# Kernel tuning notes

Hardware: AMD Instinct MI355X
Metric: run time of the kernel (lower is better)

## Reference

```python
import jax, jax.numpy as jnp
import numpy as np

FEATURE_DIM = 512
NUM_HEADS = 8
HEAD_DIM = FEATURE_DIM // NUM_HEADS


def setup_inputs() -> dict:
    key = jax.random.key(0)
    ks = jax.random.split(key, 16)
    B, N, F = 16, 768, FEATURE_DIM
    Nb = N // 3
    s = 1.0 / np.sqrt(F)
    inp = {
        "x_1": jax.random.normal(ks[0], (B, N, F), jnp.float32),
        "x_2": jax.random.normal(ks[1], (B, N, F), jnp.float32),
        "z_b": jax.random.normal(ks[2], (Nb, F), jnp.float32),
        # weights stored [in, out] (torch Linear applies x @ W.T)
        "Wqkv_i": jax.random.normal(ks[3], (F, 3 * F), jnp.float32) * s,
        "Wqkv_j": jax.random.normal(ks[4], (F, 3 * F), jnp.float32) * s,
        "Wqkv_b": jax.random.normal(ks[5], (F, 3 * F), jnp.float32) * s,
        "W_f": jax.random.normal(ks[6], (2 * F, F), jnp.float32) * s,
        "b_f": jnp.zeros((F,), jnp.float32),
        "W_m": jax.random.normal(ks[7], (F, F), jnp.float32) * s,
        "b_m": jnp.zeros((F,), jnp.float32),
        "W_QKV": jax.random.normal(ks[8], (F, 3 * F), jnp.float32) * s,
        "W_proj": jax.random.normal(ks[9], (F, F), jnp.float32) * s,
        "b_proj": jnp.zeros((F,), jnp.float32),
    }
    return inp


def reference(x_1, x_2, z_b, Wqkv_i, Wqkv_j, Wqkv_b, W_f, b_f, W_m, b_m, W_QKV, W_proj, b_proj):
    z_i, z_j = x_1, x_2
    B, N, F = z_i.shape
    Nb = z_b.shape[0]
    scale = F ** -0.5           # full-dim attention scale
    Scale = HEAD_DIM ** -0.5    # multi-head attention scale

    zb = jnp.broadcast_to((z_b * 0.2)[None], (B, Nb, F))

    def split_qkv(x, W):
        qkv = (x @ W).reshape(x.shape[0], x.shape[1], 3, F)
        return qkv[:, :, 0], qkv[:, :, 1], qkv[:, :, 2]

    _, k_i, v_i = split_qkv(z_i, Wqkv_i)
    q_j, _, _ = split_qkv(z_j, Wqkv_j)
    q_b, k_b, v_b = split_qkv(zb, Wqkv_b)

    # bottleneck cross attentions (single-head, full feature dim)
    a_ib = jax.nn.softmax(jnp.einsum('bmf,bnf->bmn', q_b, k_i) * scale, axis=-1)  # [B,Nb,N]
    a_bj = jax.nn.softmax(jnp.einsum('bnf,bmf->bnm', q_j, k_b) * scale, axis=-1)  # [B,N,Nb]

    a_ib = jnp.einsum('bmn,bnf->bmf', a_ib, v_i)  # [B,Nb,F]
    attn_up = jax.nn.softmax(jnp.einsum('bnf,bmf->bnm', z_i, a_ib) * scale, axis=-1)  # [B,N,Nb]
    a_ib = jnp.einsum('bnm,bmf->bnf', attn_up, a_ib)  # [B,N,F]
    a_bj = jnp.einsum('bnm,bmf->bnf', a_bj, v_b)      # [B,N,F]
    a_ij = (a_ib + a_bj) * 0.5

    # gated fusion
    f_ij = jax.nn.sigmoid(jnp.concatenate([a_ij, z_j], axis=-1) @ W_f + b_f)
    h_ij = jax.nn.relu(z_i + (a_ij @ W_m + b_m) * f_ij)

    # standard multi-head self-attention
    QKV = (h_ij @ W_QKV).reshape(B, N, 3, NUM_HEADS, HEAD_DIM)
    Q, K, V = [jnp.transpose(QKV[:, :, t], (0, 2, 1, 3)) for t in range(3)]  # [B,H,N,hd]
    Attn = jax.nn.softmax(jnp.einsum('bhnd,bhmd->bhnm', Q, K) * Scale, axis=-1)
    H = jnp.einsum('bhnm,bhmd->bhnd', Attn, V)
    H = jnp.transpose(H, (0, 2, 1, 3)).reshape(B, N, F)
    return H @ W_proj + b_proj
```

## Files before the change

kernel.cpp:

```cpp
#include <hip/hip_runtime.h>
#include <hip/hip_bf16.h>

typedef __attribute__((ext_vector_type(8))) short short8;
typedef __attribute__((ext_vector_type(4))) float f32x4;
typedef __hip_bfloat16 bf16;
typedef unsigned short ushort;

__device__ __forceinline__ ushort f2b(float v) {
    bf16 h = __float2bfloat16(v);
    return *reinterpret_cast<ushort*>(&h);
}
__device__ __forceinline__ float b2f(ushort u) {
    return __uint_as_float((unsigned)u << 16);
}

#define GLD16(lds, gp) __builtin_amdgcn_global_load_lds( \
    (const __attribute__((address_space(1))) void*)(gp), \
    (__attribute__((address_space(3))) void*)(lds), 16, 0, 0)

__device__ __forceinline__ void xcd_swizzle(int& bx, int& by) {
    if (gridDim.z == 1 && (gridDim.y & 7) == 0) {
        const int id = bx + gridDim.x * by;
        const int xcd = id & 7, slot = id >> 3;
        by = xcd * (gridDim.y >> 3) + slot / gridDim.x;
        bx = slot - (slot / gridDim.x) * gridDim.x;
    }
}

template<typename OutT, int EPI, int TM>
__global__ __launch_bounds__(256) void gemm_bf16(
    const bf16* __restrict__ A, const bf16* __restrict__ B, OutT* __restrict__ C,
    int K, int lda, int ldb, int ldc, long sA, long sB, long sC,
    float alpha, const float* __restrict__ bias,
    int lda2, long sA2, int eld, long sE,
    bf16* __restrict__ px, bf16* __restrict__ py)
{
    constexpr int RT = TM / 32;
    constexpr int PLA = TM * 32;
    constexpr int PLB = 128 * 32;
    constexpr int NP = (TM == 64) ? 4 : 2;
    __shared__ __align__(16) bf16 As[NP * PLA];
    __shared__ __align__(16) bf16 Bs[NP * PLB];

    const int t = threadIdx.x;
    const int w = t >> 6, lane = t & 63;
    const int wr = w >> 1, wc = w & 1;
    const int lr = lane & 15, kc4 = lane >> 4;
    const int qr = lane >> 2;
    const int kcr = ((lane & 3) - ((lane >> 3) & 3)) & 3;
    int bx = blockIdx.x, by = blockIdx.y;
    xcd_swizzle(bx, by);
    const int row0 = by * TM, col0 = bx * 128;
    const int bz = blockIdx.z;

    const bf16* Asel = A; const bf16* Bsel = B;
    int abz = bz; long sBe = sB, sAe = sA; int ldbe = ldb, ldae = lda;
    if constexpr (EPI == 7) {
        if (bz >= 16) {
            Asel = (const bf16*)px; Bsel = (const bf16*)py;
            abz = bz - 16; sBe = 0; ldbe = eld; ldae = lda2; sAe = sA2;
        }
    }
    const bf16* Ab = Asel + (size_t)abz * sAe + (size_t)row0 * ldae;
    const bf16* Bb = Bsel + (size_t)abz * sBe + (size_t)col0 * ldbe;

    const bf16* ga0; const bf16* ga1 = nullptr;
    if constexpr (TM == 64) {
        ga0 = Ab + (size_t)(w * 16 + qr) * ldae + kcr * 8;
    } else {
        ga0 = Ab + (size_t)(w * 32 + qr) * ldae + kcr * 8;
        ga1 = Ab + (size_t)(w * 32 + 16 + qr) * ldae + kcr * 8;
    }
    const bf16* gb0 = Bb + (size_t)(w * 32 + qr) * ldbe + kcr * 8;
    const bf16* gb1 = Bb + (size_t)(w * 32 + 16 + qr) * ldbe + kcr * 8;
    bf16* lA0; bf16* lA1 = nullptr;
    if constexpr (TM == 64) { lA0 = &As[w * 512]; }
    else                    { lA0 = &As[w * 1024]; lA1 = &As[w * 1024 + 512]; }
    bf16* lB0 = &Bs[w * 1024];
    bf16* lB1 = &Bs[w * 1024 + 512];

    f32x4 acc[RT][4] = {};

    const int cSw = ((kc4 + ((lr >> 1) & 3)) & 3) * 8;
    const bf16* ApBase = &As[(wr * (TM / 2) + lr) * 32 + cSw];
    const bf16* BpBase = &Bs[(wc * 64 + lr) * 32 + cSw];

    auto stageP = [&](int plane, int ko) {
        GLD16(lA0 + plane * PLA, ga0 + ko);
        if constexpr (TM == 128) GLD16(lA1 + plane * PLA, ga1 + ko);
        GLD16(lB0 + plane * PLB, gb0 + ko);
        GLD16(lB1 + plane * PLB, gb1 + ko);
    };
    auto compP = [&](int plane) {
        const bf16* Ap = ApBase + plane * PLA;
        const bf16* Bp = BpBase + plane * PLB;
        short8 af[RT], bfr[4];
#pragma unroll
        for (int i = 0; i < RT; ++i) af[i]  = *(const short8*)(Ap + i * 512);
#pragma unroll
        for (int j = 0; j < 4; ++j) bfr[j] = *(const short8*)(Bp + j * 512);
#pragma unroll
        for (int i = 0; i < RT; ++i)
#pragma unroll
            for (int j = 0; j < 4; ++j)
                acc[i][j] = __builtin_amdgcn_mfma_f32_16x16x32_bf16(af[i], bfr[j], acc[i][j], 0, 0, 0);
    };

    if constexpr (TM == 64) {
        stageP(0, 0); stageP(1, 32);
        int buf = 0;
        for (int k0 = 0; k0 < K; k0 += 64) {
            __syncthreads();
            if (k0 + 64 < K) {
                stageP((buf ^ 1) * 2,     k0 + 64);
                stageP((buf ^ 1) * 2 + 1, k0 + 96);
            }
            compP(buf * 2); compP(buf * 2 + 1);
            buf ^= 1;
        }
    } else {
        stageP(0, 0);
        int buf = 0;
        for (int k0 = 0; k0 < K; k0 += 32) {
            __syncthreads();
            if (k0 + 32 < K) stageP(buf ^ 1, k0 + 32);
            compP(buf);
            buf ^= 1;
        }
    }

    if constexpr (EPI == 4) {
        const int sec = bx >> 2;
        const int h0 = (bx & 3) * 2;
        const int b  = by / 6;
        const int n0 = (by % 6) * TM;
        bf16* dq = (bf16*)C;
#pragma unroll
        for (int j = 0; j < 4; ++j) {
            const int col = wc * 64 + j * 16 + lr;
            const int h = h0 + (col >> 6), hd = col & 63;
            const size_t bh = (size_t)b * 8 + h;
#pragma unroll
            for (int i = 0; i < RT; ++i) {
                const int n = n0 + wr * (TM / 2) + i * 16 + kc4 * 4;
                if (sec == 2) {
                    __align__(8) ushort o[4];
#pragma unroll
                    for (int r = 0; r < 4; ++r) o[r] = f2b(acc[i][j][r]);
                    *(int2*)&py[(bh * 64 + hd) * 768 + n] = *(const int2*)o;
                } else {
                    bf16* d = (sec == 0) ? dq : px;
#pragma unroll
                    for (int r = 0; r < 4; ++r)
                        d[(bh * 768 + n + r) * 64 + hd] = __float2bfloat16(acc[i][j][r]);
                }
            }
        }
        return;
    } else if constexpr (EPI == 5) {
        const int b  = by / 6;
        const int n0 = (by % 6) * TM;
#pragma unroll
        for (int j = 0; j < 4; ++j) {
            const int col = col0 + wc * 64 + j * 16 + lr;
#pragma unroll
            for (int i = 0; i < RT; ++i) {
                const int n = n0 + wr * (TM / 2) + i * 16 + kc4 * 4;
                if (col < 512) {
#pragma unroll
                    for (int r = 0; r < 4; ++r)
                        ((bf16*)C)[((size_t)b * 768 + n + r) * 512 + col] = __float2bfloat16(acc[i][j][r]);
                } else {
                    __align__(8) ushort o[4];
#pragma unroll
                    for (int r = 0; r < 4; ++r) o[r] = f2b(acc[i][j][r]);
                    *(int2*)&py[((size_t)b * 512 + (col - 512)) * 768 + n] = *(const int2*)o;
                }
            }
        }
        return;
    }

    OutT* Cb = C + (size_t)bz * sC;
#pragma unroll
    for (int j = 0; j < 4; ++j) {
        const int col = col0 + wc * 64 + j * 16 + lr;
        const float bv = bias ? bias[col] : 0.f;
#pragma unroll
        for (int i = 0; i < RT; ++i) {
            const int rb = row0 + wr * (TM / 2) + i * 16 + kc4 * 4;
            if constexpr (EPI == 6) {
                __align__(8) ushort o[4];
#pragma unroll
                for (int r = 0; r < 4; ++r) {
                    o[r] = f2b(alpha * acc[i][j][r]);
                    Cb[(size_t)(rb + r) * ldc + col] = __float2bfloat16(alpha * acc[i][j][r]);
                }
                *(int2*)&py[(size_t)bz * sE + (size_t)col * eld + rb] = *(const int2*)o;
            } else {
#pragma unroll
                for (int r = 0; r < 4; ++r) {
                    const int row = rb + r;
                    float v = alpha * acc[i][j][r] + bv;
                    if constexpr (sizeof(OutT) == 2)
                        Cb[(size_t)row * ldc + col] = __float2bfloat16(v);
                    else
                        Cb[(size_t)row * ldc + col] = v;
                }
            }
        }
    }
}

__global__ __launch_bounds__(256) void gemm_gate(
    const bf16* __restrict__ A, const bf16* __restrict__ Bf,
    const bf16* __restrict__ Bm, bf16* __restrict__ Cout,
    const float* __restrict__ bias_f, const float* __restrict__ bias_m,
    const float* __restrict__ x1)
{
    constexpr int AHW = 64 * 32;
    constexpr int BHW = 128 * 32;
    __shared__ __align__(16) bf16 As[2 * AHW];
    __shared__ __align__(16) bf16 FsS[2 * BHW];
    __shared__ __align__(16) bf16 MsS[2 * BHW];

    const int t = threadIdx.x;
    const int w = t >> 6, lane = t & 63;
    const int wr = w >> 1, wc = w & 1;
    const int lr = lane & 15, kc4 = lane >> 4;
    const int qr = lane >> 2;
    const int kcr = ((lane & 3) - ((lane >> 3) & 3)) & 3;
    int bx = blockIdx.x, by = blockIdx.y;
    xcd_swizzle(bx, by);
    const int row0 = by * 64, col0 = bx * 128;

    const bf16* ga0 = A  + (size_t)(row0 + w * 16 + qr) * 1024 + kcr * 8;
    const bf16* gf0 = Bf + (size_t)(col0 + w * 32 + qr) * 1024 + kcr * 8;
    const bf16* gf1 = Bf + (size_t)(col0 + w * 32 + 16 + qr) * 1024 + kcr * 8;
    const bf16* gm0 = Bm + (size_t)(col0 + w * 32 + qr) * 512 + kcr * 8;
    const bf16* gm1 = Bm + (size_t)(col0 + w * 32 + 16 + qr) * 512 + kcr * 8;
    bf16* lA0 = &As[w * 512];
    bf16* lF0 = &FsS[w * 1024]; bf16* lF1 = &FsS[w * 1024 + 512];
    bf16* lM0 = &MsS[w * 1024]; bf16* lM1 = &MsS[w * 1024 + 512];

    f32x4 acc1[2][4] = {};
    f32x4 acc2[2][4] = {};

    const int cSw = ((kc4 + ((lr >> 1) & 3)) & 3) * 8;
    const bf16* ApBase = &As[(wr * 32 + lr) * 32 + cSw];
    const bf16* FpBase = &FsS[(wc * 64 + lr) * 32 + cSw];
    const bf16* MpBase = &MsS[(wc * 64 + lr) * 32 + cSw];

    GLD16(lA0, ga0);
    GLD16(lF0, gf0); GLD16(lF1, gf1);
    GLD16(lM0, gm0); GLD16(lM1, gm1);

    auto step = [&](int kk, int rd, int st) {
        __syncthreads();
        const int kn = kk + 32;
        if (kn < 1024) {
            GLD16(lA0 + st * AHW, ga0 + kn);
            GLD16(lF0 + st * BHW, gf0 + kn);
            GLD16(lF1 + st * BHW, gf1 + kn);
            if (kn < 512) {
                GLD16(lM0 + st * BHW, gm0 + kn);
                GLD16(lM1 + st * BHW, gm1 + kn);
            }
        }
        const bf16* Ap = ApBase + rd * AHW;
        const bf16* Fp = FpBase + rd * BHW;
        short8 af[2], ff[4];
#pragma unroll
        for (int i = 0; i < 2; ++i) af[i] = *(const short8*)(Ap + i * 512);
#pragma unroll
        for (int j = 0; j < 4; ++j) ff[j] = *(const short8*)(Fp + j * 512);
#pragma unroll
        for (int i = 0; i < 2; ++i)
#pragma unroll
            for (int j = 0; j < 4; ++j)
                acc1[i][j] = __builtin_amdgcn_mfma_f32_16x16x32_bf16(af[i], ff[j], acc1[i][j], 0, 0, 0);
        if (kk < 512) {
            const bf16* Mp = MpBase + rd * BHW;
            short8 mf[4];
#pragma unroll
            for (int j = 0; j < 4; ++j) mf[j] = *(const short8*)(Mp + j * 512);
#pragma unroll
            for (int i = 0; i < 2; ++i)
#pragma unroll
                for (int j = 0; j < 4; ++j)
                    acc2[i][j] = __builtin_amdgcn_mfma_f32_16x16x32_bf16(af[i], mf[j], acc2[i][j], 0, 0, 0);
        }
    };

    for (int k0 = 0; k0 < 1024; k0 += 64) {
        step(k0, 0, 1);
        step(k0 + 32, 1, 0);
    }

#pragma unroll
    for (int j = 0; j < 4; ++j) {
        const int col = col0 + wc * 64 + j * 16 + lr;
        const float bvf = bias_f[col], bvm = bias_m[col];
#pragma unroll
        for (int i = 0; i < 2; ++i) {
            const int rb = row0 + wr * 32 + i * 16 + kc4 * 4;
#pragma unroll
            for (int r = 0; r < 4; ++r) {
                const int row = rb + r;
                const float sig = 1.f / (1.f + __expf(-(acc1[i][j][r] + bvf)));
                const float rr = x1[(size_t)row * 512 + col] + (acc2[i][j][r] + bvm) * sig;
                Cout[(size_t)row * 512 + col] = __float2bfloat16(rr > 0.f ? rr : 0.f);
            }
        }
    }
}

template<typename TI, int NSRC>
__global__ __launch_bounds__(256) void k_transpose(
    const TI* __restrict__ s0, const TI* __restrict__ s1,
    const TI* __restrict__ s2, const TI* __restrict__ s3,
    bf16* __restrict__ dst, int src_ld, int dst_ld, long sSrc, long sDst,
    int rep, long repStride)
{
    __shared__ float tile[64][65];
    const int t = threadIdx.x;
    const int c0 = blockIdx.x * 64, r0 = blockIdx.y * 64;
    const int z = blockIdx.z;
    const TI* src = s0;
    if (NSRC > 1) src = (z == 0) ? s0 : (z == 1) ? s1 : (z == 2) ? s2 : s3;
    {
        const int r = t >> 2, cq = (t & 3) * 16;
        const TI* sp = src + (size_t)z * sSrc + (size_t)(r0 + r) * src_ld + c0 + cq;
        if constexpr (sizeof(TI) == 4) {
#pragma unroll
            for (int u = 0; u < 16; u += 4) {
                float4 v = *(const float4*)((const float*)sp + u);
                tile[r][cq + u]     = v.x; tile[r][cq + u + 1] = v.y;
                tile[r][cq + u + 2] = v.z; tile[r][cq + u + 3] = v.w;
            }
        } else {
            const ushort* up = (const ushort*)sp;
            union { short8 v; ushort u[8]; } p0, p1;
            p0.v = *(const short8*)up; p1.v = *(const short8*)(up + 8);
#pragma unroll
            for (int u = 0; u < 8; ++u) {
                tile[r][cq + u]     = b2f(p0.u[u]);
                tile[r][cq + 8 + u] = b2f(p1.u[u]);
            }
        }
    }
    __syncthreads();
    const int c = t >> 2, rq = (t & 3) * 16;
    __align__(16) ushort ob[16];
#pragma unroll
    for (int u = 0; u < 16; ++u) ob[u] = f2b(tile[rq + u][c]);
    for (int rp = 0; rp < rep; ++rp) {
        bf16* dp = dst + (size_t)rp * repStride + (size_t)z * sDst + (size_t)(c0 + c) * dst_ld + r0 + rq;
        *(int4*)dp       = *(const int4*)&ob[0];
        *(int4*)(dp + 8) = *(const int4*)&ob[8];
    }
}

__global__ __launch_bounds__(256) void k_cast3(const float* __restrict__ x1,
    const float* __restrict__ x2, const float* __restrict__ zb,
    const float* __restrict__ wj,
    bf16* __restrict__ d1, bf16* __restrict__ d2, bf16* __restrict__ d3,
    bf16* __restrict__ d4)
{
    const int z = blockIdx.z;
    const float* src; bf16* dst; int ld; float scale; int n;
    if (z == 0)      { src = x1; dst = d1; ld = 512;  scale = 1.f;  n = 6291456; }
    else if (z == 1) { src = x2; dst = d2; ld = 1024; scale = 1.f;  n = 6291456; }
    else if (z == 2) { src = zb; dst = d3; ld = 512;  scale = 0.2f; n = 131072;  }
    else             { src = wj; dst = d4; ld = 512;  scale = 1.f;  n = 262144;  }
    int i = (blockIdx.x * 256 + threadIdx.x) * 8;
    if (i >= n) return;
    int si = i;
    if (z == 3) si = (i >> 9) * 1536 + (i & 511);
    float4 a = *(const float4*)(src + si), b = *(const float4*)(src + si + 4);
    __align__(16) ushort o[8];
    o[0] = f2b(a.x * scale); o[1] = f2b(a.y * scale); o[2] = f2b(a.z * scale); o[3] = f2b(a.w * scale);
    o[4] = f2b(b.x * scale); o[5] = f2b(b.y * scale); o[6] = f2b(b.z * scale); o[7] = f2b(b.w * scale);
    int row = i >> 9, col = i & 511;
    *(int4*)(dst + (size_t)row * ld + col) = *(const int4*)o;
}

template<int COLS, int MODE>
__global__ __launch_bounds__(256) void softmax_wave(const float* __restrict__ X,
                                                    bf16* __restrict__ Y)
{
    const int wv = threadIdx.x >> 6, lane = threadIdx.x & 63;
    const long row = (long)blockIdx.x * 4 + wv;
    const float* src = X + row * COLS;
    constexpr int V = COLS / 64;
    float v[V];
#pragma unroll
    for (int i = 0; i < V; ++i) v[i] = src[lane + i * 64];
    float m = v[0];
#pragma unroll
    for (int i = 1; i < V; ++i) m = fmaxf(m, v[i]);
#pragma unroll
    for (int o = 32; o; o >>= 1) m = fmaxf(m, __shfl_xor(m, o));
    float s = 0.f;
#pragma unroll
    for (int i = 0; i < V; ++i) { v[i] = __expf(v[i] - m); s += v[i]; }
#pragma unroll
    for (int o = 32; o; o >>= 1) s += __shfl_xor(s, o);
    const float inv = 1.f / s;
    bf16* dst;
    if constexpr (MODE == 0) {
        dst = Y + row * COLS;
    } else {
        const int z = (int)(row / 768), mm = (int)(row % 768);
        dst = Y + ((size_t)(z & 15) * 768 + mm) * 512 + (z >> 4) * 256;
    }
#pragma unroll
    for (int i = 0; i < V; ++i) dst[lane + i * 64] = __float2bfloat16(v[i] * inv);
}

__global__ __launch_bounds__(256) void mhsa_flash_mfma(
    const bf16* __restrict__ Qb, const bf16* __restrict__ Kb,
    const bf16* __restrict__ VT, bf16* __restrict__ Hout)
{
    constexpr int LD = 72;
    __shared__ __align__(16) ushort Qs[64 * LD];
    __shared__ __align__(16) ushort Ks[64 * LD];
    __shared__ __align__(16) ushort Vt[64 * LD];
    __shared__ __align__(16) ushort Ps[64 * LD];

    const int t = threadIdx.x;
    const int w = t >> 6, lane = t & 63;
    const int l16 = lane & 15, q4 = lane >> 4;
    const int h = blockIdx.x, b = blockIdx.y, qt = blockIdx.z;
    const size_t bh = (size_t)b * 8 + h;
    const ushort* qbase = (const ushort*)Qb + bh * 768 * 64;
    const ushort* kbase = (const ushort*)Kb + bh * 768 * 64;
    const ushort* vbase = (const ushort*)VT + bh * 64 * 768;

    const int r = t >> 2, c0 = (t & 3) * 16;

    {
        const ushort* src = qbase + (size_t)(qt * 64 + r) * 64 + c0;
        *(int4*)&Qs[r * LD + c0]     = *(const int4*)src;
        *(int4*)&Qs[r * LD + c0 + 8] = *(const int4*)(src + 8);
    }

    int4 ka0, ka1, va0, va1;
    {
        const ushort* ks = kbase + (size_t)r * 64 + c0;
        ka0 = *(const int4*)ks; ka1 = *(const int4*)(ks + 8);
        const ushort* vs = vbase + (size_t)r * 768 + c0;
        va0 = *(const int4*)vs; va1 = *(const int4*)(vs + 8);
    }
    __syncthreads();

    short8 qf0 = *(const short8*)&Qs[(w * 16 + l16) * LD + q4 * 8];
    short8 qf1 = *(const short8*)&Qs[(w * 16 + l16) * LD + 32 + q4 * 8];

    float lsum[4] = {0.f, 0.f, 0.f, 0.f};
    f32x4 acc[4] = {};

    for (int kt = 0; kt < 12; ++kt) {
        if (kt) __syncthreads();
        *(int4*)&Ks[r * LD + c0]     = ka0;
        *(int4*)&Ks[r * LD + c0 + 8] = ka1;
        *(int4*)&Vt[r * LD + c0]     = va0;
        *(int4*)&Vt[r * LD + c0 + 8] = va1;
        __syncthreads();

        if (kt < 11) {
            const ushort* ks = kbase + (size_t)((kt + 1) * 64 + r) * 64 + c0;
            ka0 = *(const int4*)ks; ka1 = *(const int4*)(ks + 8);
            const ushort* vs = vbase + (size_t)r * 768 + (kt + 1) * 64 + c0;
            va0 = *(const int4*)vs; va1 = *(const int4*)(vs + 8);
        }

        f32x4 s[4] = {};
#pragma unroll
        for (int nt = 0; nt < 4; ++nt) {
            short8 kf0 = *(const short8*)&Ks[(nt * 16 + l16) * LD + q4 * 8];
            short8 kf1 = *(const short8*)&Ks[(nt * 16 + l16) * LD + 32 + q4 * 8];
            s[nt] = __builtin_amdgcn_mfma_f32_16x16x32_bf16(qf0, kf0, s[nt], 0, 0, 0);
            s[nt] = __builtin_amdgcn_mfma_f32_16x16x32_bf16(qf1, kf1, s[nt], 0, 0, 0);
        }

#pragma unroll
        for (int nt = 0; nt < 4; ++nt) {
#pragma unroll
            for (int e = 0; e < 4; ++e) {
                const float p = __expf(s[nt][e] * 0.125f);
                lsum[e] += p;
                Ps[(w * 16 + q4 * 4 + e) * LD + nt * 16 + l16] = f2b(p);
            }
        }

        short8 pf0 = *(const short8*)&Ps[(w * 16 + l16) * LD + q4 * 8];
        short8 pf1 = *(const short8*)&Ps[(w * 16 + l16) * LD + 32 + q4 * 8];
#pragma unroll
        for (int jt = 0; jt < 4; ++jt) {
            short8 vf0 = *(const short8*)&Vt[(jt * 16 + l16) * LD + q4 * 8];
            short8 vf1 = *(const short8*)&Vt[(jt * 16 + l16) * LD + 32 + q4 * 8];
            acc[jt] = __builtin_amdgcn_mfma_f32_16x16x32_bf16(pf0, vf0, acc[jt], 0, 0, 0);
            acc[jt] = __builtin_amdgcn_mfma_f32_16x16x32_bf16(pf1, vf1, acc[jt], 0, 0, 0);
        }
    }

    const int orow = qt * 64 + w * 16 + q4 * 4;
#pragma unroll
    for (int e = 0; e < 4; ++e) {
        float l = lsum[e];
        l += __shfl_xor(l, 1);
        l += __shfl_xor(l, 2);
        l += __shfl_xor(l, 4);
        l += __shfl_xor(l, 8);
        const float inv = 1.f / l;
        const size_t rbase = ((size_t)b * 768 + orow + e) * 512 + h * 64;
#pragma unroll
        for (int jt = 0; jt < 4; ++jt)
            Hout[rbase + jt * 16 + l16] = __float2bfloat16(acc[jt][e] * inv);
    }
}

extern "C" void kernel_launch(void* const* d_in, const int* in_sizes, int n_in,
                              void* d_out, int out_size, void* d_ws, size_t ws_size,
                              hipStream_t stream)
{
    (void)in_sizes; (void)n_in; (void)out_size; (void)ws_size;
    const float* x1     = (const float*)d_in[0];
    const float* x2     = (const float*)d_in[1];
    const float* z_b    = (const float*)d_in[2];
    const float* Wqkv_i = (const float*)d_in[3];
    const float* Wqkv_j = (const float*)d_in[4];
    const float* Wqkv_b = (const float*)d_in[5];
    const float* W_f    = (const float*)d_in[6];
    const float* b_f    = (const float*)d_in[7];
    const float* W_m    = (const float*)d_in[8];
    const float* b_m    = (const float*)d_in[9];
    const float* W_QKV  = (const float*)d_in[10];
    const float* W_proj = (const float*)d_in[11];
    const float* b_proj = (const float*)d_in[12];
    float* out = (float*)d_out;

    const float scale = 0.044194173824159216f;

    char* base = (char*)d_ws;
    size_t off = 0;
    auto alloc = [&](size_t bytes) { char* r = base + off; off += (bytes + 255) & ~(size_t)255; return r; };

    char* Rq  = alloc((size_t)3 * 25165824);
    char* R1  = Rq;
    char* R2  = Rq + 25165824;
    char* R3  = Rq + 2 * 25165824;
    char* R4  = alloc(25165824);
    bf16* Wt4     = (bf16*)alloc((size_t)3 * 1536 * 512 * 2);
    bf16* Wt_f    = (bf16*)alloc(512 * 1024 * 2);
    bf16* Wt_mp   = (bf16*)alloc((size_t)2 * 512 * 512 * 2);
    bf16* Wj_bf   = (bf16*)alloc(512 * 512 * 2);
    bf16* Gbuf    = (bf16*)alloc(256 * 512 * 2);
    bf16* c_zb    = (bf16*)alloc(256 * 512 * 2);
    bf16* qkvb    = (bf16*)alloc(256 * 1536 * 2);
    bf16* aib0    = (bf16*)alloc((size_t)16 * 256 * 512 * 2);
    bf16* Bcat    = (bf16*)alloc((size_t)16 * 512 * 512 * 2);
    float* S      = (float*)alloc((size_t)32 * 768 * 256 * 4);
    bf16* Sb1     = (bf16*)alloc((size_t)16 * 256 * 768 * 2);
    bf16* Sb_cat  = (bf16*)alloc((size_t)16 * 768 * 512 * 2);
    bf16* c_cat   = (bf16*)alloc((size_t)12288 * 1024 * 2);
    bf16* hbuf    = (bf16*)alloc((size_t)12288 * 512 * 2);

    bf16* Wt_i = Wt4, *Wt_b = Wt4 + 1536 * 512,
        *Wt_qkv = Wt4 + (size_t)2 * 1536 * 512;
    bf16* Wt_m = Wt_mp, *Wt_proj = Wt_mp + 512 * 512;

    bf16*  Kc   = (bf16*)R1;
    bf16*  Qb   = (bf16*)R1;
    bf16*  Kb   = (bf16*)(R1 + 12582912);
    bf16*  v_iT = (bf16*)R2;
    bf16*  VTb  = (bf16*)R2;
    bf16*  c_x1 = (bf16*)R3;
    bf16*  Hout = (bf16*)R4;

    auto G64 = [&](const bf16* A, const bf16* B, void* C, bool outBf,
                   int M, int N, int K, int lda, int ldb, int ldc,
                   long sA, long sB, long sC, int batch, float alpha, const float* bias) {
        dim3 grid(N / 128, M / 64, batch);
        if (outBf) gemm_bf16<bf16, 0, 64><<<grid, 256, 0, stream>>>(A, B, (bf16*)C, K, lda, ldb, ldc, sA, sB, sC, alpha, bias, 0, 0, 0, 0, nullptr, nullptr);
        else       gemm_bf16<float, 0, 64><<<grid, 256, 0, stream>>>(A, B, (float*)C, K, lda, ldb, ldc, sA, sB, sC, alpha, bias, 0, 0, 0, 0, nullptr, nullptr);
    };

    k_cast3<<<dim3(3072, 1, 4), 256, 0, stream>>>(x1, x2, z_b, Wqkv_j,
                                                  c_x1, c_cat + 512, c_zb, Wj_bf);
    k_transpose<float, 3><<<dim3(24, 8, 3), 256, 0, stream>>>(
        Wqkv_i, Wqkv_b, W_QKV, nullptr, Wt4, 1536, 512, 0, 1536L * 512, 1, 0);
    k_transpose<float, 1><<<dim3(8, 16, 1), 256, 0, stream>>>(
        W_f, nullptr, nullptr, nullptr, Wt_f, 512, 1024, 0, 0, 1, 0);
    k_transpose<float, 2><<<dim3(8, 8, 2), 256, 0, stream>>>(
        W_m, W_proj, nullptr, nullptr, Wt_mp, 512, 512, 0, 512L * 512, 1, 0);

    G64(c_zb, Wt_b, qkvb, true, 256, 1536, 512, 512, 512, 1536, 0, 0, 0, 1, 1.f, nullptr);
    G64(qkvb + 512, Wj_bf, Gbuf, true, 256, 512, 512, 1536, 512, 512, 0, 0, 0, 1, 1.f, nullptr);
    k_transpose<bf16, 1><<<dim3(8, 4, 1), 256, 0, stream>>>(
        qkvb + 1024, nullptr, nullptr, nullptr, Bcat + 256, 1536, 512, 0, 0, 16, 512L * 512);
    gemm_bf16<bf16, 5, 128><<<dim3(8, 96, 1), 256, 0, stream>>>(
        c_x1, Wt_i + 512 * 512, Kc, 512, 512, 512, 512, 0, 0, 0,
        1.f, nullptr, 0, 0, 0, 0, nullptr, v_iT);
    G64(qkvb, Kc, S, false, 256, 768, 512, 1536, 512, 768, 0, 768L * 512, 256L * 768, 16, scale, nullptr);
    softmax_wave<768, 0><<<1024, 256, 0, stream>>>(S, Sb1);
    gemm_bf16<bf16, 6, 64><<<dim3(4, 4, 16), 256, 0, stream>>>(
        Sb1, v_iT, aib0, 768, 768, 768, 512, 256L * 768, 512L * 768, 256L * 512,
        1.f, nullptr, 0, 0, 512, 512L * 512, nullptr, Bcat);
    gemm_bf16<float, 7, 64><<<dim3(2, 12, 32), 256, 0, stream>>>(
        c_x1, aib0, S, 512, 512, 512, 256, 768L * 512, 256L * 512, 768L * 256,
        scale, nullptr, 1024, 768L * 1024, 512, 0,
        c_cat + 512, Gbuf);
    softmax_wave<256, 1><<<6144, 256, 0, stream>>>(S, Sb_cat);
    G64(Sb_cat, Bcat, c_cat, true, 768, 512, 512, 512, 512, 1024,
        768L * 512, 512L * 512, 768L * 1024, 16, 0.5f, nullptr);
    gemm_gate<<<dim3(4, 192), 256, 0, stream>>>(c_cat, Wt_f, Wt_m, hbuf, b_f, b_m, x1);
    gemm_bf16<bf16, 4, 128><<<dim3(12, 96, 1), 256, 0, stream>>>(
        hbuf, Wt_qkv, Qb, 512, 512, 512, 0, 0, 0, 0,
        1.f, nullptr, 0, 0, 0, 0, Kb, VTb);
    mhsa_flash_mfma<<<dim3(8, 16, 12), 256, 0, stream>>>(Qb, Kb, VTb, Hout);
    G64(Hout, Wt_proj, out, false, 12288, 512, 512, 512, 512, 512, 0, 0, 0, 1, 1.f, b_proj);
}
```

Before: 380.1 us.

## Fold batch into grid y for XCD swizzle, fuse v_b transpose, reshape gate warps

Batched GEMMs now fold the batch index into gridDim.y (passing rows-per-batch as nry), so the XCD swizzle also applies to batched launches and spreads batches across chiplets for L2 locality. The q/k/v_b projection gets a new epilogue (EPI 8) that writes the transposed v_b slice into Bcat for all 16 batches directly, which removes a separate transpose kernel. The gated GEMM's warp tiling changes from a 2x2 warp grid to 1x4, so each warp owns 64 rows by 32 columns. The extra replicated stores in the fused epilogue and the larger A-fragment load per warp are the trade-offs.

```diff
diff --git a/kernel.cpp b/kernel.cpp
--- a/kernel.cpp
+++ b/kernel.cpp
@@ -19,7 +19,7 @@
     (__attribute__((address_space(3))) void*)(lds), 16, 0, 0)
 
 __device__ __forceinline__ void xcd_swizzle(int& bx, int& by) {
-    if (gridDim.z == 1 && (gridDim.y & 7) == 0) {
+    if ((gridDim.y & 7) == 0) {
         const int id = bx + gridDim.x * by;
         const int xcd = id & 7, slot = id >> 3;
         by = xcd * (gridDim.y >> 3) + slot / gridDim.x;
@@ -33,7 +33,7 @@
     int K, int lda, int ldb, int ldc, long sA, long sB, long sC,
     float alpha, const float* __restrict__ bias,
     int lda2, long sA2, int eld, long sE,
-    bf16* __restrict__ px, bf16* __restrict__ py)
+    bf16* __restrict__ px, bf16* __restrict__ py, int nry)
 {
     constexpr int RT = TM / 32;
     constexpr int PLA = TM * 32;
@@ -50,19 +50,21 @@
     const int kcr = ((lane & 3) - ((lane >> 3) & 3)) & 3;
     int bx = blockIdx.x, by = blockIdx.y;
     xcd_swizzle(bx, by);
-    const int row0 = by * TM, col0 = bx * 128;
-    const int bz = blockIdx.z;
+    int zidx, row0;
+    if (nry > 0) { zidx = by / nry; row0 = (by % nry) * TM; }
+    else         { zidx = blockIdx.z; row0 = by * TM; }
+    const int col0 = bx * 128;
 
     const bf16* Asel = A; const bf16* Bsel = B;
-    int abz = bz; long sBe = sB, sAe = sA; int ldbe = ldb, ldae = lda;
+    long sBe = sB, sAe = sA; int ldbe = ldb, ldae = lda;
     if constexpr (EPI == 7) {
-        if (bz >= 16) {
+        if (blockIdx.z == 1) {
             Asel = (const bf16*)px; Bsel = (const bf16*)py;
-            abz = bz - 16; sBe = 0; ldbe = eld; ldae = lda2; sAe = sA2;
-        }
-    }
-    const bf16* Ab = Asel + (size_t)abz * sAe + (size_t)row0 * ldae;
-    const bf16* Bb = Bsel + (size_t)abz * sBe + (size_t)col0 * ldbe;
+            sBe = 0; ldbe = eld; ldae = lda2; sAe = sA2;
+        }
+    }
+    const bf16* Ab = Asel + (size_t)zidx * sAe + (size_t)row0 * ldae;
+    const bf16* Bb = Bsel + (size_t)zidx * sBe + (size_t)col0 * ldbe;
 
     const bf16* ga0; const bf16* ga1 = nullptr;
     if constexpr (TM == 64) {
@@ -181,7 +183,8 @@
         return;
     }
 
-    OutT* Cb = C + (size_t)bz * sC;
+    const int czid = (EPI == 7) ? (int)blockIdx.z * 16 + zidx : zidx;
+    OutT* Cb = C + (size_t)czid * sC;
 #pragma unroll
     for (int j = 0; j < 4; ++j) {
         const int col = col0 + wc * 64 + j * 16 + lr;
@@ -196,7 +199,20 @@
                     o[r] = f2b(alpha * acc[i][j][r]);
                     Cb[(size_t)(rb + r) * ldc + col] = __float2bfloat16(alpha * acc[i][j][r]);
                 }
-                *(int2*)&py[(size_t)bz * sE + (size_t)col * eld + rb] = *(const int2*)o;
+                *(int2*)&py[(size_t)czid * sE + (size_t)col * eld + rb] = *(const int2*)o;
+            } else if constexpr (EPI == 8) {
+                __align__(8) ushort o[4];
+#pragma unroll
+                for (int r = 0; r < 4; ++r) {
+                    o[r] = f2b(acc[i][j][r]);
+                    Cb[(size_t)(rb + r) * ldc + col] = __float2bfloat16(acc[i][j][r]);
+                }
+                if (col >= 1024) {
+                    const size_t tb = (size_t)(col - 1024) * 512 + 256 + rb;
+#pragma unroll
+                    for (int b2 = 0; b2 < 16; ++b2)
+                        *(int2*)&py[(size_t)b2 * sE + tb] = *(const int2*)o;
+                }
             } else {
 #pragma unroll
                 for (int r = 0; r < 4; ++r) {
@@ -226,7 +242,6 @@
 
     const int t = threadIdx.x;
     const int w = t >> 6, lane = t & 63;
-    const int wr = w >> 1, wc = w & 1;
     const int lr = lane & 15, kc4 = lane >> 4;
     const int qr = lane >> 2;
     const int kcr = ((lane & 3) - ((lane >> 3) & 3)) & 3;
@@ -243,13 +258,13 @@
     bf16* lF0 = &FsS[w * 1024]; bf16* lF1 = &FsS[w * 1024 + 512];
     bf16* lM0 = &MsS[w * 1024]; bf16* lM1 = &MsS[w * 1024 + 512];
 
-    f32x4 acc1[2][4] = {};
-    f32x4 acc2[2][4] = {};
+    f32x4 acc1[4][2] = {};
+    f32x4 acc2[4][2] = {};
 
     const int cSw = ((kc4 + ((lr >> 1) & 3)) & 3) * 8;
-    const bf16* ApBase = &As[(wr * 32 + lr) * 32 + cSw];
-    const bf16* FpBase = &FsS[(wc * 64 + lr) * 32 + cSw];
-    const bf16* MpBase = &MsS[(wc * 64 + lr) * 32 + cSw];
+    const bf16* ApBase = &As[lr * 32 + cSw];
+    const bf16* FpBase = &FsS[(w * 32 + lr) * 32 + cSw];
+    const bf16* MpBase = &MsS[(w * 32 + lr) * 32 + cSw];
 
     GLD16(lA0, ga0);
     GLD16(lF0, gf0); GLD16(lF1, gf1);
@@ -269,25 +284,25 @@
         }
         const bf16* Ap = ApBase + rd * AHW;
         const bf16* Fp = FpBase + rd * BHW;
-        short8 af[2], ff[4];
-#pragma unroll
-        for (int i = 0; i < 2; ++i) af[i] = *(const short8*)(Ap + i * 512);
-#pragma unroll
-        for (int j = 0; j < 4; ++j) ff[j] = *(const short8*)(Fp + j * 512);
-#pragma unroll
-        for (int i = 0; i < 2; ++i)
-#pragma unroll
-            for (int j = 0; j < 4; ++j)
+        short8 af[4], ff[2];
+#pragma unroll
+        for (int i = 0; i < 4; ++i) af[i] = *(const short8*)(Ap + i * 512);
+#pragma unroll
+        for (int j = 0; j < 2; ++j) ff[j] = *(const short8*)(Fp + j * 512);
+#pragma unroll
+        for (int i = 0; i < 4; ++i)
+#pragma unroll
+            for (int j = 0; j < 2; ++j)
                 acc1[i][j] = __builtin_amdgcn_mfma_f32_16x16x32_bf16(af[i], ff[j], acc1[i][j], 0, 0, 0);
         if (kk < 512) {
             const bf16* Mp = MpBase + rd * BHW;
-            short8 mf[4];
-#pragma unroll
-            for (int j = 0; j < 4; ++j) mf[j] = *(const short8*)(Mp + j * 512);
-#pragma unroll
-            for (int i = 0; i < 2; ++i)
-#pragma unroll
-                for (int j = 0; j < 4; ++j)
+            short8 mf[2];
+#pragma unroll
+            for (int j = 0; j < 2; ++j) mf[j] = *(const short8*)(Mp + j * 512);
+#pragma unroll
+            for (int i = 0; i < 4; ++i)
+#pragma unroll
+                for (int j = 0; j < 2; ++j)
                     acc2[i][j] = __builtin_amdgcn_mfma_f32_16x16x32_bf16(af[i], mf[j], acc2[i][j], 0, 0, 0);
         }
     };
@@ -298,12 +313,12 @@
     }
 
 #pragma unroll
-    for (int j = 0; j < 4; ++j) {
-        const int col = col0 + wc * 64 + j * 16 + lr;
+    for (int j = 0; j < 2; ++j) {
+        const int col = col0 + w * 32 + j * 16 + lr;
         const float bvf = bias_f[col], bvm = bias_m[col];
 #pragma unroll
-        for (int i = 0; i < 2; ++i) {
-            const int rb = row0 + wr * 32 + i * 16 + kc4 * 4;
+        for (int i = 0; i < 4; ++i) {
+            const int rb = row0 + i * 16 + kc4 * 4;
 #pragma unroll
             for (int r = 0; r < 4; ++r) {
                 const int row = rb + r;
@@ -581,10 +596,13 @@
 
     auto G64 = [&](const bf16* A, const bf16* B, void* C, bool outBf,
                    int M, int N, int K, int lda, int ldb, int ldc,
-                   long sA, long sB, long sC, int batch, float alpha, const float* bias) {
-        dim3 grid(N / 128, M / 64, batch);
-        if (outBf) gemm_bf16<bf16, 0, 64><<<grid, 256, 0, stream>>>(A, B, (bf16*)C, K, lda, ldb, ldc, sA, sB, sC, alpha, bias, 0, 0, 0, 0, nullptr, nullptr);
-        else       gemm_bf16<float, 0, 64><<<grid, 256, 0, stream>>>(A, B, (float*)C, K, lda, ldb, ldc, sA, sB, sC, alpha, bias, 0, 0, 0, 0, nullptr, nullptr);
+                   long sA, long sB, long sC, int batch, float alpha,
+                   const float* bias) {
+        int nry = M / 64;
+        dim3 grid(N / 128, (batch > 1) ? batch * nry : nry, 1);
+        if (batch == 1) nry = 0;
+        if (outBf) gemm_bf16<bf16, 0, 64><<<grid, 256, 0, stream>>>(A, B, (bf16*)C, K, lda, ldb, ldc, sA, sB, sC, alpha, bias, 0, 0, 0, 0, nullptr, nullptr, nry);
+        else       gemm_bf16<float, 0, 64><<<grid, 256, 0, stream>>>(A, B, (float*)C, K, lda, ldb, ldc, sA, sB, sC, alpha, bias, 0, 0, 0, 0, nullptr, nullptr, nry);
     };
 
     k_cast3<<<dim3(3072, 1, 4), 256, 0, stream>>>(x1, x2, z_b, Wqkv_j,
@@ -596,29 +614,29 @@
     k_transpose<float, 2><<<dim3(8, 8, 2), 256, 0, stream>>>(
         W_m, W_proj, nullptr, nullptr, Wt_mp, 512, 512, 0, 512L * 512, 1, 0);
 
-    G64(c_zb, Wt_b, qkvb, true, 256, 1536, 512, 512, 512, 1536, 0, 0, 0, 1, 1.f, nullptr);
+    gemm_bf16<bf16, 8, 64><<<dim3(12, 4, 1), 256, 0, stream>>>(
+        c_zb, Wt_b, qkvb, 512, 512, 512, 1536, 0, 0, 0,
+        1.f, nullptr, 0, 0, 0, 512L * 512, nullptr, Bcat, 0);
     G64(qkvb + 512, Wj_bf, Gbuf, true, 256, 512, 512, 1536, 512, 512, 0, 0, 0, 1, 1.f, nullptr);
-    k_transpose<bf16, 1><<<dim3(8, 4, 1), 256, 0, stream>>>(
-        qkvb + 1024, nullptr, nullptr, nullptr, Bcat + 256, 1536, 512, 0, 0, 16, 512L * 512);
     gemm_bf16<bf16, 5, 128><<<dim3(8, 96, 1), 256, 0, stream>>>(
         c_x1, Wt_i + 512 * 512, Kc, 512, 512, 512, 512, 0, 0, 0,
-        1.f, nullptr, 0, 0, 0, 0, nullptr, v_iT);
+        1.f, nullptr, 0, 0, 0, 0, nullptr, v_iT, 0);
     G64(qkvb, Kc, S, false, 256, 768, 512, 1536, 512, 768, 0, 768L * 512, 256L * 768, 16, scale, nullptr);
     softmax_wave<768, 0><<<1024, 256, 0, stream>>>(S, Sb1);
-    gemm_bf16<bf16, 6, 64><<<dim3(4, 4, 16), 256, 0, stream>>>(
+    gemm_bf16<bf16, 6, 64><<<dim3(4, 64, 1), 256, 0, stream>>>(
         Sb1, v_iT, aib0, 768, 768, 768, 512, 256L * 768, 512L * 768, 256L * 512,
-        1.f, nullptr, 0, 0, 512, 512L * 512, nullptr, Bcat);
-    gemm_bf16<float, 7, 64><<<dim3(2, 12, 32), 256, 0, stream>>>(
+        1.f, nullptr, 0, 0, 512, 512L * 512, nullptr, Bcat, 4);
+    gemm_bf16<float, 7, 64><<<dim3(2, 192, 2), 256, 0, stream>>>(
         c_x1, aib0, S, 512, 512, 512, 256, 768L * 512, 256L * 512, 768L * 256,
         scale, nullptr, 1024, 768L * 1024, 512, 0,
-        c_cat + 512, Gbuf);
+        c_cat + 512, Gbuf, 12);
     softmax_wave<256, 1><<<6144, 256, 0, stream>>>(S, Sb_cat);
     G64(Sb_cat, Bcat, c_cat, true, 768, 512, 512, 512, 512, 1024,
         768L * 512, 512L * 512, 768L * 1024, 16, 0.5f, nullptr);
     gemm_gate<<<dim3(4, 192), 256, 0, stream>>>(c_cat, Wt_f, Wt_m, hbuf, b_f, b_m, x1);
     gemm_bf16<bf16, 4, 128><<<dim3(12, 96, 1), 256, 0, stream>>>(
         hbuf, Wt_qkv, Qb, 512, 512, 512, 0, 0, 0, 0,
-        1.f, nullptr, 0, 0, 0, 0, Kb, VTb);
+        1.f, nullptr, 0, 0, 0, 0, Kb, VTb, 0);
     mhsa_flash_mfma<<<dim3(8, 16, 12), 256, 0, stream>>>(Qb, Kb, VTb, Hout);
     G64(Hout, Wt_proj, out, false, 12288, 512, 512, 512, 512, 512, 0, 0, 0, 1, 1.f, b_proj);
 }
```

Measured after the change: 382.4 us. No clear change (+0.6%).
